# Kernel optimization log

Hardware: AMD Instinct MI355X
Metric: run time of the kernel (lower is better)

Reference implementation:

```python
import jax, jax.numpy as jnp
import numpy as np

B, N, E = 8, 512, 65536          # graphs per batch, nodes per graph, total edges
D_IN, D_H = 128, 64              # psi_1 in/out channels
R_IN, R_OUT = 32, 32             # psi_2 in/out channels (rnd indicator dim)
STEPS = 2                        # num consensus steps
NT = B * N                       # total nodes


def _gnn(x, src, dst, ea, W_root, W_nbr, b):
    """Edge-weighted GraphConv: relu(x W_root + A_w x W_nbr + b)."""
    msg = x[src] * ea                                    # [E, F] gather + scale
    agg = jax.ops.segment_sum(msg, dst, num_segments=NT)  # scatter-add
    return jax.nn.relu(x @ W_root + agg @ W_nbr + b)


def setup_inputs() -> dict:
    key = jax.random.key(0)
    ks = jax.random.split(key, 16)
    off = jnp.repeat(jnp.arange(B, dtype=jnp.int32) * N, E // B)  # keep edges within graphs

    def edges(k):
        k1, k2 = jax.random.split(k)
        src = jax.random.randint(k1, (E,), 0, N) + off
        dst = jax.random.randint(k2, (E,), 0, N) + off
        return jnp.stack([src, dst]).astype(jnp.int32)

    s = 0.1
    inp = {
        "x_s": jax.random.normal(ks[0], (NT, D_IN), jnp.float32),
        "edge_index_s": edges(ks[1]),
        "edge_attr_s": jax.random.uniform(ks[2], (E, 1), jnp.float32),
        "batch_s": jnp.repeat(jnp.arange(B, dtype=jnp.int32), N),
        "x_t": jax.random.normal(ks[3], (NT, D_IN), jnp.float32),
        "edge_index_t": edges(ks[4]),
        "edge_attr_t": jax.random.uniform(ks[5], (E, 1), jnp.float32),
        "batch_t": jnp.repeat(jnp.arange(B, dtype=jnp.int32), N),
        "r_s_all": jax.random.normal(ks[6], (STEPS, B, N, R_IN), jnp.float32),
        # psi_1 params
        "W1_root": jax.random.normal(ks[7], (D_IN, D_H), jnp.float32) * s,
        "W1_nbr": jax.random.normal(ks[8], (D_IN, D_H), jnp.float32) * s,
        "b1": jnp.zeros((D_H,), jnp.float32),
        # psi_2 params
        "W2_root": jax.random.normal(ks[9], (R_IN, R_OUT), jnp.float32) * s,
        "W2_nbr": jax.random.normal(ks[10], (R_IN, R_OUT), jnp.float32) * s,
        "b2": jnp.zeros((R_OUT,), jnp.float32),
        # consensus MLP: Lin(R_OUT,R_OUT) -> ReLU -> Lin(R_OUT,1)
        "Wm1": jax.random.normal(ks[11], (R_OUT, R_OUT), jnp.float32) * s,
        "bm1": jnp.zeros((R_OUT,), jnp.float32),
        "Wm2": jax.random.normal(ks[12], (R_OUT, 1), jnp.float32) * s,
        "bm2": jnp.zeros((1,), jnp.float32),
    }
    return inp


def reference(x_s, edge_index_s, edge_attr_s, batch_s,
              x_t, edge_index_t, edge_attr_t, batch_t, r_s_all,
              W1_root, W1_nbr, b1, W2_root, W2_nbr, b2,
              Wm1, bm1, Wm2, bm2):
    src_s, dst_s = edge_index_s[0], edge_index_s[1]
    src_t, dst_t = edge_index_t[0], edge_index_t[1]

    # psi_1: local matching embeddings
    h_s = _gnn(x_s, src_s, dst_s, edge_attr_s, W1_root, W1_nbr, b1)
    h_t = _gnn(x_t, src_t, dst_t, edge_attr_t, W1_root, W1_nbr, b1)

    # to_dense_batch: graphs are equal-sized (batch = repeat(arange(B), N)),
    # so dense batching is a reshape and all node masks are True ->
    # masked_softmax reduces to plain softmax (masked_fill is a no-op).
    h_s = h_s.reshape(B, N, D_H)
    h_t = h_t.reshape(B, N, D_H)

    S_hat0 = jnp.einsum('bsd,btd->bst', h_s, h_t)  # [B, N, N]
    S_0 = jax.nn.softmax(S_hat0, axis=-1)

    def mlp(D):  # D: [B, N, N, R_OUT] -> [B, N, N]
        h = jax.nn.relu(D @ Wm1 + bm1)
        return (h @ Wm2 + bm2)[..., 0]

    def step(S_hat, r_s):
        S = jax.nn.softmax(S_hat, axis=-1)
        r_t = jnp.einsum('bst,bsr->btr', S, r_s)        # S^T @ r_s
        o_s = _gnn(r_s.reshape(NT, R_IN), src_s, dst_s, edge_attr_s,
                   W2_root, W2_nbr, b2).reshape(B, N, R_OUT)
        o_t = _gnn(r_t.reshape(NT, R_IN), src_t, dst_t, edge_attr_t,
                   W2_root, W2_nbr, b2).reshape(B, N, R_OUT)
        D = o_s[:, :, None, :] - o_t[:, None, :, :]     # [B, N, N, R_OUT]
        return S_hat + mlp(D), None

    S_hat, _ = jax.lax.scan(step, S_hat0, r_s_all)
    S_L = jax.nn.softmax(S_hat, axis=-1)
    return (S_0, S_L)
```

## Files before the change

kernel.cpp:

```cpp
#include <hip/hip_runtime.h>

constexpr int B = 8, N = 512, E = 65536;
constexpr int D_IN = 128, D_H = 64, R_IN = 32, R_OUT = 32;
constexpr int NT = B * N;
constexpr size_t NN = (size_t)B * N * N;
constexpr int CAP = 64;

__global__ __launch_bounds__(256) void setup_pack(
    const int* __restrict__ src_s, const int* __restrict__ dst_s,
    const float* __restrict__ ea_s,
    const int* __restrict__ src_t, const int* __restrict__ dst_t,
    const float* __restrict__ ea_t,
    int* __restrict__ deg, int2* __restrict__ pack_s, int2* __restrict__ pack_t,
    const float* __restrict__ x_s, const float* __restrict__ x_t,
    const float* __restrict__ Wr, const float* __restrict__ Wn,
    const float* __restrict__ b,
    float* __restrict__ xr, float* __restrict__ xn) {
  __shared__ float smem[32 * D_IN + D_IN * 128];
  const int bid = blockIdx.x;
  const int tid = threadIdx.x;

  if (bid < 512) {
    const int gid = bid * 256 + tid;
    const int side = gid >> 16;
    const int e = gid & (E - 1);
    const int* __restrict__ src = side ? src_t : src_s;
    const int* __restrict__ dst = side ? dst_t : dst_s;
    const float* __restrict__ ea = side ? ea_t : ea_s;
    int2* __restrict__ pack = side ? pack_t : pack_s;
    const int d = dst[e];
    const int slot = atomicAdd(&deg[side * NT + d], 1);
    if (slot < CAP)
      pack[((size_t)d << 6) + slot] = make_int2(src[e], __float_as_int(ea[e]));
    return;
  }

  float (*xls)[D_IN] = (float(*)[D_IN])smem;
  float (*Wb)[128]   = (float(*)[128])(smem + 32 * D_IN);
  const int pb = bid - 512;
  const int side = pb >> 7;
  const int n0 = (pb & 127) * 32;
  const float* __restrict__ x = side ? x_t : x_s;

#pragma unroll
  for (int j = 0; j < 4; ++j) {
    const int i = tid + j * 256;
    const int n = i >> 5, k4 = (i & 31) * 4;
    *(float4*)&xls[n][k4] = *(const float4*)(x + (size_t)(n0 + n) * D_IN + k4);
  }
#pragma unroll
  for (int j = 0; j < 8; ++j) {
    const int i = tid + j * 256;
    const int k = i >> 4, c4 = (i & 15) * 4;
    *(float4*)&Wb[k][c4]      = *(const float4*)(Wr + k * D_H + c4);
    *(float4*)&Wb[k][64 + c4] = *(const float4*)(Wn + k * D_H + c4);
  }
  __syncthreads();

  const int c0 = (tid & 31) * 4;
  const int nb = (tid >> 5) * 4;
  float4 bv = make_float4(0.f, 0.f, 0.f, 0.f);
  if (c0 < 64) bv = *(const float4*)(b + c0);
  float4 acc0 = bv, acc1 = bv, acc2 = bv, acc3 = bv;

#pragma unroll 16
  for (int k = 0; k < D_IN; ++k) {
    const float4 w = *(const float4*)&Wb[k][c0];
    const float x0 = xls[nb + 0][k];
    const float x1 = xls[nb + 1][k];
    const float x2 = xls[nb + 2][k];
    const float x3 = xls[nb + 3][k];
    acc0.x += x0 * w.x; acc0.y += x0 * w.y; acc0.z += x0 * w.z; acc0.w += x0 * w.w;
    acc1.x += x1 * w.x; acc1.y += x1 * w.y; acc1.z += x1 * w.z; acc1.w += x1 * w.w;
    acc2.x += x2 * w.x; acc2.y += x2 * w.y; acc2.z += x2 * w.z; acc2.w += x2 * w.w;
    acc3.x += x3 * w.x; acc3.y += x3 * w.y; acc3.z += x3 * w.z; acc3.w += x3 * w.w;
  }

  const size_t gbase = (size_t)(side * NT + n0 + nb);
  if (c0 < 64) {
    *(float4*)(xr + (gbase + 0) * D_H + c0) = acc0;
    *(float4*)(xr + (gbase + 1) * D_H + c0) = acc1;
    *(float4*)(xr + (gbase + 2) * D_H + c0) = acc2;
    *(float4*)(xr + (gbase + 3) * D_H + c0) = acc3;
  } else {
    const int c = c0 - 64;
    *(float4*)(xn + (gbase + 0) * D_H + c) = acc0;
    *(float4*)(xn + (gbase + 1) * D_H + c) = acc1;
    *(float4*)(xn + (gbase + 2) * D_H + c) = acc2;
    *(float4*)(xn + (gbase + 3) * D_H + c) = acc3;
  }
}

__global__ __launch_bounds__(256) void agg_pack(
    const float* __restrict__ xn, const int* __restrict__ deg,
    const int2* __restrict__ pack_s, const int2* __restrict__ pack_t,
    float* __restrict__ ag,
    const float* __restrict__ r_all,
    const float* __restrict__ W2r, const float* __restrict__ W2n,
    const float* __restrict__ b2,
    const float* __restrict__ Wm1, const float* __restrict__ bm1,
    float* __restrict__ Psb) {
  __shared__ float sh[3 * 8 * 33];
  const int bid = blockIdx.x;
  const int tid = threadIdx.x;

  if (bid < 512) {
    const int gid = bid * 256 + tid;
    const int side = gid >> 16;
    const int local = gid & 65535;
    const int n = local >> 4;
    const int c4 = (local & 15) * 4;
    const int2* __restrict__ pack = side ? pack_t : pack_s;
    const float* __restrict__ xb = xn + (size_t)side * NT * D_H;
    const int cnt = deg[side * NT + n];
    const size_t base = (size_t)n << 6;
    float4 acc = make_float4(0.f, 0.f, 0.f, 0.f);
    for (int k = 0; k < cnt; ++k) {
      const int2 p = pack[base + k];
      const float w = __int_as_float(p.y);
      const float4 v = *(const float4*)(xb + (size_t)p.x * D_H + c4);
      acc.x += v.x * w; acc.y += v.y * w; acc.z += v.z * w; acc.w += v.w * w;
    }
    *(float4*)(ag + ((size_t)side * NT + n) * D_H + c4) = acc;
    return;
  }

  float (*agg)[33] = (float(*)[33])sh;
  float (*rr)[33]  = (float(*)[33])(sh + 8 * 33);
  float (*o)[33]   = (float(*)[33])(sh + 16 * 33);
  const int blk = bid - 512;
  const int st = blk >> 9;
  const int n0 = (blk & 511) * 8;
  const float* __restrict__ r = r_all + (size_t)st * NT * R_IN;
  const int g = tid >> 5, j = tid & 31;
  const int n = n0 + g;
  const int cnt = deg[n];
  const size_t base = (size_t)n << 6;
  float acc = 0.f;
  for (int k = 0; k < cnt; ++k) {
    const int2 p = pack_s[base + k];
    acc += r[(size_t)p.x * R_IN + j] * __int_as_float(p.y);
  }
  agg[g][j] = acc;
  rr[g][j] = r[(size_t)n * R_IN + j];
  __syncthreads();
  float v = b2[j];
#pragma unroll 8
  for (int k = 0; k < 32; ++k)
    v += rr[g][k] * W2r[k * 32 + j] + agg[g][k] * W2n[k * 32 + j];
  o[g][j] = fmaxf(v, 0.f);
  __syncthreads();
  float p2 = bm1[j];
#pragma unroll 8
  for (int k = 0; k < 32; ++k) p2 += o[g][k] * Wm1[k * 32 + j];
  Psb[((size_t)st * NT + n) * 32 + j] = p2;
}

__global__ void gemm_sm(const float* __restrict__ xr_all, const float* __restrict__ ag_all,
                        float* __restrict__ Shat, float* __restrict__ S0) {
  __shared__ float hs[16][65];
  __shared__ float ht[256][65];
  const int b = blockIdx.x >> 5;
  const int s0 = (blockIdx.x & 31) * 16;
  const int tid = threadIdx.x;
  const int sg = tid >> 6;
  const int tg = tid & 63;

  {
    const int r = tid >> 4, c4 = (tid & 15) * 4;
    const size_t idx = ((size_t)(b * N + s0 + r)) * D_H + c4;
    const float4 a1 = *(const float4*)(xr_all + idx);
    const float4 a2 = *(const float4*)(ag_all + idx);
    hs[r][c4 + 0] = fmaxf(a1.x + a2.x, 0.f);
    hs[r][c4 + 1] = fmaxf(a1.y + a2.y, 0.f);
    hs[r][c4 + 2] = fmaxf(a1.z + a2.z, 0.f);
    hs[r][c4 + 3] = fmaxf(a1.w + a2.w, 0.f);
  }
  const float* __restrict__ xr_t = xr_all + (size_t)NT * D_H;
  const float* __restrict__ ag_t = ag_all + (size_t)NT * D_H;

  float l[2][4][4];
#pragma unroll
  for (int ch = 0; ch < 2; ++ch) {
    __syncthreads();
#pragma unroll
    for (int jj = 0; jj < 16; ++jj) {
      const int i = tid + jj * 256;
      const int r = i >> 4, c4 = (i & 15) * 4;
      const size_t idx = ((size_t)(b * N + ch * 256 + r)) * D_H + c4;
      const float4 v1 = *(const float4*)(xr_t + idx);
      const float4 v2 = *(const float4*)(ag_t + idx);
      ht[r][c4 + 0] = fmaxf(v1.x + v2.x, 0.f);
      ht[r][c4 + 1] = fmaxf(v1.y + v2.y, 0.f);
      ht[r][c4 + 2] = fmaxf(v1.z + v2.z, 0.f);
      ht[r][c4 + 3] = fmaxf(v1.w + v2.w, 0.f);
    }
    __syncthreads();
    float a[4][4];
#pragma unroll
    for (int j = 0; j < 4; ++j)
#pragma unroll
      for (int i = 0; i < 4; ++i) a[j][i] = 0.f;
#pragma unroll 8
    for (int k = 0; k < D_H; ++k) {
      const float t0v = ht[tg][k];
      const float t1v = ht[tg + 64][k];
      const float t2v = ht[tg + 128][k];
      const float t3v = ht[tg + 192][k];
#pragma unroll
      for (int i = 0; i < 4; ++i) {
        const float h = hs[sg * 4 + i][k];
        a[0][i] += h * t0v;
        a[1][i] += h * t1v;
        a[2][i] += h * t2v;
        a[3][i] += h * t3v;
      }
    }
#pragma unroll
    for (int j = 0; j < 4; ++j)
#pragma unroll
      for (int i = 0; i < 4; ++i) l[ch][j][i] = a[j][i];
  }

  float m[4], inv[4];
#pragma unroll
  for (int i = 0; i < 4; ++i) {
    float mm = -3.4e38f;
#pragma unroll
    for (int ch = 0; ch < 2; ++ch)
#pragma unroll
      for (int j = 0; j < 4; ++j) mm = fmaxf(mm, l[ch][j][i]);
#pragma unroll
    for (int o = 32; o; o >>= 1) mm = fmaxf(mm, __shfl_xor(mm, o));
    m[i] = mm;
  }
#pragma unroll
  for (int i = 0; i < 4; ++i) {
    float ss = 0.f;
#pragma unroll
    for (int ch = 0; ch < 2; ++ch)
#pragma unroll
      for (int j = 0; j < 4; ++j) ss += __expf(l[ch][j][i] - m[i]);
#pragma unroll
    for (int o = 32; o; o >>= 1) ss += __shfl_xor(ss, o);
    inv[i] = 1.0f / ss;
  }
#pragma unroll
  for (int i = 0; i < 4; ++i) {
    const size_t rowb = ((size_t)b * N + s0 + sg * 4 + i) * N;
#pragma unroll
    for (int ch = 0; ch < 2; ++ch)
#pragma unroll
      for (int j = 0; j < 4; ++j) {
        const int t = ch * 256 + j * 64 + tg;
        const float lv = l[ch][j][i];
        Shat[rowb + t] = lv;
        S0[rowb + t] = __expf(lv - m[i]) * inv[i];
      }
  }
}

template <int STATS>
__global__ void rt_part_k(const float* __restrict__ Sdata,
                          const float* __restrict__ rowM, const float* __restrict__ rowInv,
                          const float* __restrict__ rs, float* __restrict__ part) {
  __shared__ float Ss[32][33];
  __shared__ float Rs[32][32];
  const int b = blockIdx.z;
  const int sq = blockIdx.y;
  const int t0 = blockIdx.x * 32;
  const float* Sb = Sdata + (size_t)b * N * N;
  const float* rb = rs + (size_t)b * N * R_IN;
  const int tid = threadIdx.x;
  const int lt = tid >> 3;
  const int r0 = (tid & 7) * 4;
  float a0 = 0, a1 = 0, a2 = 0, a3 = 0;
  for (int c = 0; c < 4; ++c) {
    const int s0 = sq * 128 + c * 32;
    for (int i = tid; i < 1024; i += 256) {
      const int ss = i >> 5, cc = i & 31;
      float v = Sb[(size_t)(s0 + ss) * N + t0 + cc];
      if (STATS) {
        const int grow = b * N + s0 + ss;
        v = __expf(v - rowM[grow]) * rowInv[grow];
      }
      Ss[ss][cc] = v;
      Rs[ss][cc] = rb[(size_t)(s0 + ss) * R_IN + cc];
    }
    __syncthreads();
#pragma unroll 8
    for (int ss = 0; ss < 32; ++ss) {
      const float sv = Ss[ss][lt];
      a0 += sv * Rs[ss][r0 + 0];
      a1 += sv * Rs[ss][r0 + 1];
      a2 += sv * Rs[ss][r0 + 2];
      a3 += sv * Rs[ss][r0 + 3];
    }
    __syncthreads();
  }
  float4* out = (float4*)(part + ((size_t)sq * NT + b * N + t0 + lt) * R_IN + r0);
  *out = make_float4(a0, a1, a2, a3);
}

__global__ void gp2t(const float* __restrict__ part,
                     const int* __restrict__ degp, const int2* __restrict__ pack,
                     const float* __restrict__ W2r, const float* __restrict__ W2n,
                     const float* __restrict__ b2,
                     const float* __restrict__ Wm1, const float* __restrict__ bm1,
                     float* __restrict__ Pout) {
  __shared__ float ag[8][33], rr[8][33], o[8][33];
  const int n0 = blockIdx.x * 8;
  const int g = threadIdx.x >> 5, j = threadIdx.x & 31;
  const int n = n0 + g;
  const int cnt = degp[n];
  const size_t base = (size_t)n << 6;
  const size_t P = (size_t)NT * R_IN;
  float acc = 0.f;
  for (int k = 0; k < cnt; ++k) {
    const int2 p = pack[base + k];
    const size_t ri = (size_t)p.x * R_IN + j;
    const float rv = ((part[ri] + part[P + ri]) + part[2 * P + ri]) + part[3 * P + ri];
    acc += rv * __int_as_float(p.y);
  }
  ag[g][j] = acc;
  {
    const size_t ri = (size_t)n * R_IN + j;
    rr[g][j] = ((part[ri] + part[P + ri]) + part[2 * P + ri]) + part[3 * P + ri];
  }
  __syncthreads();
  float v = b2[j];
#pragma unroll 8
  for (int k = 0; k < 32; ++k)
    v += rr[g][k] * W2r[k * 32 + j] + ag[g][k] * W2n[k * 32 + j];
  o[g][j] = fmaxf(v, 0.f);
  __syncthreads();
  float p2 = 0.f;
#pragma unroll 8
  for (int k = 0; k < 32; ++k) p2 += o[g][k] * Wm1[k * 32 + j];
  Pout[(size_t)n * 32 + j] = p2;
}

template <int LAST>
__global__ void update_sm2(const float* __restrict__ Ps, const float* __restrict__ Pt,
                           const float* __restrict__ Wm2, const float* __restrict__ bm2,
                           float* __restrict__ Shat, float* __restrict__ S,
                           float* __restrict__ rowM, float* __restrict__ rowInv) {
  __shared__ float pt4[128][36];
  const int row0 = blockIdx.x * 8;
  const int b = row0 >> 9;
  const int tid = threadIdx.x;
  const int s_loc = tid >> 5;
  const int lane_t = tid & 31;
  const int row = row0 + s_loc;

  float ps[32], w2v[32];
#pragma unroll
  for (int q = 0; q < 8; ++q) {
    const float4 v = *(const float4*)(Ps + (size_t)row * 32 + q * 4);
    ps[q * 4 + 0] = v.x; ps[q * 4 + 1] = v.y; ps[q * 4 + 2] = v.z; ps[q * 4 + 3] = v.w;
    const float4 w = *(const float4*)(Wm2 + q * 4);
    w2v[q * 4 + 0] = w.x; w2v[q * 4 + 1] = w.y; w2v[q * 4 + 2] = w.z; w2v[q * 4 + 3] = w.w;
  }
  const float bb = bm2[0];

  float l[16];
#pragma unroll
  for (int c = 0; c < 4; ++c) {
    __syncthreads();
#pragma unroll
    for (int j = 0; j < 4; ++j) {
      const int i = tid + j * 256;
      const int t = i >> 3, k4 = (i & 7) * 4;
      const float4 v = *(const float4*)(Pt + ((size_t)(b * N) + c * 128 + t) * 32 + k4);
      *(float4*)&pt4[t][k4] = v;
    }
    __syncthreads();
#pragma unroll
    for (int q = 0; q < 4; ++q) {
      const int tq = q * 32 + lane_t;
      float d = 0.f;
#pragma unroll
      for (int k4 = 0; k4 < 8; ++k4) {
        const float4 pv = *(const float4*)&pt4[tq][k4 * 4];
        d += fmaxf(ps[k4 * 4 + 0] - pv.x, 0.f) * w2v[k4 * 4 + 0];
        d += fmaxf(ps[k4 * 4 + 1] - pv.y, 0.f) * w2v[k4 * 4 + 1];
        d += fmaxf(ps[k4 * 4 + 2] - pv.z, 0.f) * w2v[k4 * 4 + 2];
        d += fmaxf(ps[k4 * 4 + 3] - pv.w, 0.f) * w2v[k4 * 4 + 3];
      }
      const int t = c * 128 + q * 32 + lane_t;
      l[c * 4 + q] = Shat[(size_t)row * N + t] + d + bb;
    }
  }

  float m = l[0];
#pragma unroll
  for (int i = 1; i < 16; ++i) m = fmaxf(m, l[i]);
#pragma unroll
  for (int o = 16; o; o >>= 1) m = fmaxf(m, __shfl_xor(m, o));
  float sum = 0.f;
#pragma unroll
  for (int i = 0; i < 16; ++i) sum += __expf(l[i] - m);
#pragma unroll
  for (int o = 16; o; o >>= 1) sum += __shfl_xor(sum, o);
  const float inv = 1.0f / sum;

  if (!LAST) {
#pragma unroll
    for (int c = 0; c < 4; ++c)
#pragma unroll
      for (int q = 0; q < 4; ++q) {
        const int t = c * 128 + q * 32 + lane_t;
        Shat[(size_t)row * N + t] = l[c * 4 + q];
      }
    if (lane_t == 0) { rowM[row] = m; rowInv[row] = inv; }
  } else {
#pragma unroll
    for (int c = 0; c < 4; ++c)
#pragma unroll
      for (int q = 0; q < 4; ++q) {
        const int t = c * 128 + q * 32 + lane_t;
        S[(size_t)row * N + t] = __expf(l[c * 4 + q] - m) * inv;
      }
  }
}

extern "C" void kernel_launch(void* const* d_in, const int* in_sizes, int n_in,
                              void* d_out, int out_size, void* d_ws, size_t ws_size,
                              hipStream_t stream) {
  const float* x_s  = (const float*)d_in[0];
  const int*   ei_s = (const int*)d_in[1];
  const float* ea_s = (const float*)d_in[2];
  const float* x_t  = (const float*)d_in[4];
  const int*   ei_t = (const int*)d_in[5];
  const float* ea_t = (const float*)d_in[6];
  const float* r_all = (const float*)d_in[8];
  const float* W1r = (const float*)d_in[9];
  const float* W1n = (const float*)d_in[10];
  const float* b1  = (const float*)d_in[11];
  const float* W2r = (const float*)d_in[12];
  const float* W2n = (const float*)d_in[13];
  const float* b2  = (const float*)d_in[14];
  const float* Wm1 = (const float*)d_in[15];
  const float* bm1 = (const float*)d_in[16];
  const float* Wm2 = (const float*)d_in[17];
  const float* bm2 = (const float*)d_in[18];

  const int* src_s = ei_s;
  const int* dst_s = ei_s + E;
  const int* src_t = ei_t;
  const int* dst_t = ei_t + E;

  float* ws = (float*)d_ws;
  float* xr   = ws; ws += (size_t)2 * NT * D_H;
  float* xn   = ws; ws += (size_t)2 * NT * D_H;
  float* ag   = ws; ws += (size_t)2 * NT * D_H;
  float* Shat = ws; ws += NN;
  float* rt_p = ws; ws += (size_t)4 * NT * R_IN;
  float* Psb  = ws; ws += (size_t)2 * NT * R_OUT;
  float* Ptb  = ws; ws += (size_t)NT * R_OUT;
  float* rowM = ws; ws += NT;
  float* rowI = ws; ws += NT;
  int* deg      = (int*)ws; ws += 2 * NT;
  int2* pack_s  = (int2*)ws; ws += (size_t)NT * CAP * 2;
  int2* pack_t  = (int2*)ws; ws += (size_t)NT * CAP * 2;

  float* S0_out = (float*)d_out;
  float* SL_out = S0_out + NN;

  hipMemsetAsync(deg, 0, 2 * NT * sizeof(int), stream);
  setup_pack<<<768, 256, 0, stream>>>(src_s, dst_s, ea_s, src_t, dst_t, ea_t,
                                      deg, pack_s, pack_t,
                                      x_s, x_t, W1r, W1n, b1, xr, xn);
  agg_pack<<<1536, 256, 0, stream>>>(xn, deg, pack_s, pack_t, ag,
                                     r_all, W2r, W2n, b2, Wm1, bm1, Psb);
  gemm_sm<<<256, 256, 0, stream>>>(xr, ag, Shat, S0_out);

  rt_part_k<0><<<dim3(16, 4, B), 256, 0, stream>>>(S0_out, nullptr, nullptr, r_all, rt_p);
  gp2t<<<512, 256, 0, stream>>>(rt_p, deg + NT, pack_t, W2r, W2n, b2, Wm1, bm1, Ptb);
  update_sm2<0><<<512, 256, 0, stream>>>(Psb, Ptb, Wm2, bm2, Shat, nullptr, rowM, rowI);

  rt_part_k<1><<<dim3(16, 4, B), 256, 0, stream>>>(Shat, rowM, rowI,
                                                   r_all + (size_t)NT * R_IN, rt_p);
  gp2t<<<512, 256, 0, stream>>>(rt_p, deg + NT, pack_t, W2r, W2n, b2, Wm1, bm1, Ptb);
  update_sm2<1><<<512, 256, 0, stream>>>(Psb + (size_t)NT * R_OUT, Ptb, Wm2, bm2,
                                         Shat, SL_out, nullptr, nullptr);
}
```

Measured before the change: 231.5 us.

## Fuse h activation into aggregation, widen gemm blocks, split r_t reduction and stage in LDS

The agg_pack kernel now adds the root term and applies ReLU, writing the finished h once so gemm_sm loads it directly instead of re-reading two buffers and recomputing relu. gemm_sm runs 512 threads per block, each handling 2 rows instead of 4, which roughly halves per-thread register use. The S^T r partial products are split into 8 chunks instead of 4 to raise parallelism, and a separate reduce kernel sums them. gp2t then stages the whole graph's r_t rows and edge packs in shared memory for its gather. The cost is an extra kernel launch per step and more partial-buffer traffic.

```diff
diff --git a/kernel.cpp b/kernel.cpp
--- a/kernel.cpp
+++ b/kernel.cpp
@@ -92,9 +92,10 @@
 }
 
 __global__ __launch_bounds__(256) void agg_pack(
-    const float* __restrict__ xn, const int* __restrict__ deg,
+    const float* __restrict__ xn, const float* __restrict__ xr,
+    const int* __restrict__ deg,
     const int2* __restrict__ pack_s, const int2* __restrict__ pack_t,
-    float* __restrict__ ag,
+    float* __restrict__ h,
     const float* __restrict__ r_all,
     const float* __restrict__ W2r, const float* __restrict__ W2n,
     const float* __restrict__ b2,
@@ -121,7 +122,10 @@
       const float4 v = *(const float4*)(xb + (size_t)p.x * D_H + c4);
       acc.x += v.x * w; acc.y += v.y * w; acc.z += v.z * w; acc.w += v.w * w;
     }
-    *(float4*)(ag + ((size_t)side * NT + n) * D_H + c4) = acc;
+    const size_t oi = ((size_t)side * NT + n) * D_H + c4;
+    const float4 rv = *(const float4*)(xr + oi);
+    *(float4*)(h + oi) = make_float4(fmaxf(rv.x + acc.x, 0.f), fmaxf(rv.y + acc.y, 0.f),
+                                     fmaxf(rv.z + acc.z, 0.f), fmaxf(rv.w + acc.w, 0.f));
     return;
   }
 
@@ -156,8 +160,9 @@
   Psb[((size_t)st * NT + n) * 32 + j] = p2;
 }
 
-__global__ void gemm_sm(const float* __restrict__ xr_all, const float* __restrict__ ag_all,
-                        float* __restrict__ Shat, float* __restrict__ S0) {
+__global__ __launch_bounds__(512) void gemm_sm(const float* __restrict__ h,
+                                               float* __restrict__ Shat,
+                                               float* __restrict__ S0) {
   __shared__ float hs[16][65];
   __shared__ float ht[256][65];
   const int b = blockIdx.x >> 5;
@@ -165,66 +170,52 @@
   const int tid = threadIdx.x;
   const int sg = tid >> 6;
   const int tg = tid & 63;
-
-  {
+  const float* __restrict__ h_t = h + (size_t)NT * D_H;
+
+  if (tid < 256) {
     const int r = tid >> 4, c4 = (tid & 15) * 4;
-    const size_t idx = ((size_t)(b * N + s0 + r)) * D_H + c4;
-    const float4 a1 = *(const float4*)(xr_all + idx);
-    const float4 a2 = *(const float4*)(ag_all + idx);
-    hs[r][c4 + 0] = fmaxf(a1.x + a2.x, 0.f);
-    hs[r][c4 + 1] = fmaxf(a1.y + a2.y, 0.f);
-    hs[r][c4 + 2] = fmaxf(a1.z + a2.z, 0.f);
-    hs[r][c4 + 3] = fmaxf(a1.w + a2.w, 0.f);
-  }
-  const float* __restrict__ xr_t = xr_all + (size_t)NT * D_H;
-  const float* __restrict__ ag_t = ag_all + (size_t)NT * D_H;
-
-  float l[2][4][4];
+    *(float4*)&hs[r][c4] =
+        *(const float4*)(h + ((size_t)(b * N + s0 + r)) * D_H + c4);
+  }
+
+  float l[2][4][2];
 #pragma unroll
   for (int ch = 0; ch < 2; ++ch) {
     __syncthreads();
 #pragma unroll
-    for (int jj = 0; jj < 16; ++jj) {
-      const int i = tid + jj * 256;
+    for (int jj = 0; jj < 8; ++jj) {
+      const int i = tid + jj * 512;
       const int r = i >> 4, c4 = (i & 15) * 4;
-      const size_t idx = ((size_t)(b * N + ch * 256 + r)) * D_H + c4;
-      const float4 v1 = *(const float4*)(xr_t + idx);
-      const float4 v2 = *(const float4*)(ag_t + idx);
-      ht[r][c4 + 0] = fmaxf(v1.x + v2.x, 0.f);
-      ht[r][c4 + 1] = fmaxf(v1.y + v2.y, 0.f);
-      ht[r][c4 + 2] = fmaxf(v1.z + v2.z, 0.f);
-      ht[r][c4 + 3] = fmaxf(v1.w + v2.w, 0.f);
-    }
-    __syncthreads();
-    float a[4][4];
-#pragma unroll
-    for (int j = 0; j < 4; ++j)
-#pragma unroll
-      for (int i = 0; i < 4; ++i) a[j][i] = 0.f;
+      *(float4*)&ht[r][c4] =
+          *(const float4*)(h_t + ((size_t)(b * N + ch * 256 + r)) * D_H + c4);
+    }
+    __syncthreads();
+    float a[4][2];
+#pragma unroll
+    for (int j = 0; j < 4; ++j) { a[j][0] = 0.f; a[j][1] = 0.f; }
 #pragma unroll 8
     for (int k = 0; k < D_H; ++k) {
       const float t0v = ht[tg][k];
       const float t1v = ht[tg + 64][k];
       const float t2v = ht[tg + 128][k];
       const float t3v = ht[tg + 192][k];
-#pragma unroll
-      for (int i = 0; i < 4; ++i) {
-        const float h = hs[sg * 4 + i][k];
-        a[0][i] += h * t0v;
-        a[1][i] += h * t1v;
-        a[2][i] += h * t2v;
-        a[3][i] += h * t3v;
-      }
-    }
-#pragma unroll
-    for (int j = 0; j < 4; ++j)
-#pragma unroll
-      for (int i = 0; i < 4; ++i) l[ch][j][i] = a[j][i];
-  }
-
-  float m[4], inv[4];
-#pragma unroll
-  for (int i = 0; i < 4; ++i) {
+      const float h0 = hs[sg * 2 + 0][k];
+      const float h1 = hs[sg * 2 + 1][k];
+      a[0][0] += h0 * t0v; a[0][1] += h1 * t0v;
+      a[1][0] += h0 * t1v; a[1][1] += h1 * t1v;
+      a[2][0] += h0 * t2v; a[2][1] += h1 * t2v;
+      a[3][0] += h0 * t3v; a[3][1] += h1 * t3v;
+    }
+#pragma unroll
+    for (int j = 0; j < 4; ++j) {
+      l[ch][j][0] = a[j][0];
+      l[ch][j][1] = a[j][1];
+    }
+  }
+
+  float m[2], inv[2];
+#pragma unroll
+  for (int i = 0; i < 2; ++i) {
     float mm = -3.4e38f;
 #pragma unroll
     for (int ch = 0; ch < 2; ++ch)
@@ -235,7 +226,7 @@
     m[i] = mm;
   }
 #pragma unroll
-  for (int i = 0; i < 4; ++i) {
+  for (int i = 0; i < 2; ++i) {
     float ss = 0.f;
 #pragma unroll
     for (int ch = 0; ch < 2; ++ch)
@@ -246,8 +237,8 @@
     inv[i] = 1.0f / ss;
   }
 #pragma unroll
-  for (int i = 0; i < 4; ++i) {
-    const size_t rowb = ((size_t)b * N + s0 + sg * 4 + i) * N;
+  for (int i = 0; i < 2; ++i) {
+    const size_t rowb = ((size_t)b * N + s0 + sg * 2 + i) * N;
 #pragma unroll
     for (int ch = 0; ch < 2; ++ch)
 #pragma unroll
@@ -275,8 +266,8 @@
   const int lt = tid >> 3;
   const int r0 = (tid & 7) * 4;
   float a0 = 0, a1 = 0, a2 = 0, a3 = 0;
-  for (int c = 0; c < 4; ++c) {
-    const int s0 = sq * 128 + c * 32;
+  for (int c = 0; c < 2; ++c) {
+    const int s0 = sq * 64 + c * 32;
     for (int i = tid; i < 1024; i += 256) {
       const int ss = i >> 5, cc = i & 31;
       float v = Sb[(size_t)(s0 + ss) * N + t0 + cc];
@@ -302,31 +293,49 @@
   *out = make_float4(a0, a1, a2, a3);
 }
 
-__global__ void gp2t(const float* __restrict__ part,
-                     const int* __restrict__ degp, const int2* __restrict__ pack,
-                     const float* __restrict__ W2r, const float* __restrict__ W2n,
-                     const float* __restrict__ b2,
-                     const float* __restrict__ Wm1, const float* __restrict__ bm1,
-                     float* __restrict__ Pout) {
+__global__ void rt_reduce8(const float* __restrict__ part, float* __restrict__ rt) {
+  const size_t i = ((size_t)blockIdx.x * 256 + threadIdx.x) * 4;
+  float4 a = *(const float4*)(part + i);
+#pragma unroll
+  for (int p = 1; p < 8; ++p) {
+    const float4 v = *(const float4*)(part + (size_t)p * NT * R_IN + i);
+    a.x += v.x; a.y += v.y; a.z += v.z; a.w += v.w;
+  }
+  *(float4*)(rt + i) = a;
+}
+
+__global__ __launch_bounds__(256) void gp2t(
+    const float* __restrict__ rt_b,
+    const int* __restrict__ degp, const int2* __restrict__ pack,
+    const float* __restrict__ W2r, const float* __restrict__ W2n,
+    const float* __restrict__ b2,
+    const float* __restrict__ Wm1, const float* __restrict__ bm1,
+    float* __restrict__ Pout) {
+  __shared__ float rtb[512][32];
+  __shared__ int2 pck[512];
   __shared__ float ag[8][33], rr[8][33], o[8][33];
   const int n0 = blockIdx.x * 8;
-  const int g = threadIdx.x >> 5, j = threadIdx.x & 31;
+  const int bb = n0 >> 9;
+  const int tid = threadIdx.x;
+
+  for (int i = tid; i < 4096; i += 256) {
+    const int row = i >> 3, k4 = (i & 7) * 4;
+    *(float4*)&rtb[row][k4] =
+        *(const float4*)(rt_b + ((size_t)(bb * N) + row) * R_IN + k4);
+  }
+  for (int i = tid; i < 512; i += 256) pck[i] = pack[(size_t)n0 * CAP + i];
+  __syncthreads();
+
+  const int g = tid >> 5, j = tid & 31;
   const int n = n0 + g;
   const int cnt = degp[n];
-  const size_t base = (size_t)n << 6;
-  const size_t P = (size_t)NT * R_IN;
   float acc = 0.f;
   for (int k = 0; k < cnt; ++k) {
-    const int2 p = pack[base + k];
-    const size_t ri = (size_t)p.x * R_IN + j;
-    const float rv = ((part[ri] + part[P + ri]) + part[2 * P + ri]) + part[3 * P + ri];
-    acc += rv * __int_as_float(p.y);
+    const int2 p = pck[g * CAP + k];
+    acc += rtb[p.x & 511][j] * __int_as_float(p.y);
   }
   ag[g][j] = acc;
-  {
-    const size_t ri = (size_t)n * R_IN + j;
-    rr[g][j] = ((part[ri] + part[P + ri]) + part[2 * P + ri]) + part[3 * P + ri];
-  }
+  rr[g][j] = rtb[n & 511][j];
   __syncthreads();
   float v = b2[j];
 #pragma unroll 8
@@ -453,9 +462,10 @@
   float* ws = (float*)d_ws;
   float* xr   = ws; ws += (size_t)2 * NT * D_H;
   float* xn   = ws; ws += (size_t)2 * NT * D_H;
-  float* ag   = ws; ws += (size_t)2 * NT * D_H;
+  float* h    = ws; ws += (size_t)2 * NT * D_H;
   float* Shat = ws; ws += NN;
-  float* rt_p = ws; ws += (size_t)4 * NT * R_IN;
+  float* rt_p = ws; ws += (size_t)8 * NT * R_IN;
+  float* rt_b = ws; ws += (size_t)NT * R_IN;
   float* Psb  = ws; ws += (size_t)2 * NT * R_OUT;
   float* Ptb  = ws; ws += (size_t)NT * R_OUT;
   float* rowM = ws; ws += NT;
@@ -471,17 +481,19 @@
   setup_pack<<<768, 256, 0, stream>>>(src_s, dst_s, ea_s, src_t, dst_t, ea_t,
                                       deg, pack_s, pack_t,
                                       x_s, x_t, W1r, W1n, b1, xr, xn);
-  agg_pack<<<1536, 256, 0, stream>>>(xn, deg, pack_s, pack_t, ag,
+  agg_pack<<<1536, 256, 0, stream>>>(xn, xr, deg, pack_s, pack_t, h,
                                      r_all, W2r, W2n, b2, Wm1, bm1, Psb);
-  gemm_sm<<<256, 256, 0, stream>>>(xr, ag, Shat, S0_out);
-
-  rt_part_k<0><<<dim3(16, 4, B), 256, 0, stream>>>(S0_out, nullptr, nullptr, r_all, rt_p);
-  gp2t<<<512, 256, 0, stream>>>(rt_p, deg + NT, pack_t, W2r, W2n, b2, Wm1, bm1, Ptb);
+  gemm_sm<<<256, 512, 0, stream>>>(h, Shat, S0_out);
+
+  rt_part_k<0><<<dim3(16, 8, B), 256, 0, stream>>>(S0_out, nullptr, nullptr, r_all, rt_p);
+  rt_reduce8<<<128, 256, 0, stream>>>(rt_p, rt_b);
+  gp2t<<<512, 256, 0, stream>>>(rt_b, deg + NT, pack_t, W2r, W2n, b2, Wm1, bm1, Ptb);
   update_sm2<0><<<512, 256, 0, stream>>>(Psb, Ptb, Wm2, bm2, Shat, nullptr, rowM, rowI);
 
-  rt_part_k<1><<<dim3(16, 4, B), 256, 0, stream>>>(Shat, rowM, rowI,
+  rt_part_k<1><<<dim3(16, 8, B), 256, 0, stream>>>(Shat, rowM, rowI,
                                                    r_all + (size_t)NT * R_IN, rt_p);
-  gp2t<<<512, 256, 0, stream>>>(rt_p, deg + NT, pack_t, W2r, W2n, b2, Wm1, bm1, Ptb);
+  rt_reduce8<<<128, 256, 0, stream>>>(rt_p, rt_b);
+  gp2t<<<512, 256, 0, stream>>>(rt_b, deg + NT, pack_t, W2r, W2n, b2, Wm1, bm1, Ptb);
   update_sm2<1><<<512, 256, 0, stream>>>(Psb + (size_t)NT * R_OUT, Ptb, Wm2, bm2,
                                          Shat, SL_out, nullptr, nullptr);
 }
```

Result: faster. 200.3 us, median of 2 (-13.5%).
